# Performance work log

Hardware: AMD Instinct MI355X
Metric: run time of the kernel (lower is better)

## Reference

```python
import jax, jax.numpy as jnp
import numpy as np

B, L, D = 1, 512, 768
INIT_STD = 0.02


def setup_inputs() -> dict:
    key = jax.random.key(0)
    ks = jax.random.split(key, 6)
    hidden_states = jax.random.normal(ks[0], (B, L, D), dtype=jnp.float32)
    attention_mask = jnp.zeros((B, 1, L), dtype=jnp.float32)  # additive mask
    # nn.Linear weights, stored as [in, out] so forward is x @ W + b
    Wq = jax.random.normal(ks[1], (D, D), dtype=jnp.float32) * INIT_STD
    bq = jnp.zeros((D,), dtype=jnp.float32)
    Wk = jax.random.normal(ks[2], (D, D), dtype=jnp.float32) * INIT_STD
    bk = jnp.zeros((D,), dtype=jnp.float32)
    w_att = jax.random.normal(ks[3], (D,), dtype=jnp.float32) * INIT_STD  # Linear(D,1)
    b_att = jnp.zeros((), dtype=jnp.float32)
    Wt = jax.random.normal(ks[4], (D, D), dtype=jnp.float32) * INIT_STD
    bt = jnp.zeros((D,), dtype=jnp.float32)
    return {
        "hidden_states": hidden_states,
        "attention_mask": attention_mask,
        "Wq": Wq, "bq": bq, "Wk": Wk, "bk": bk,
        "w_att": w_att, "b_att": b_att, "Wt": Wt, "bt": bt,
    }


def reference(hidden_states, attention_mask, Wq, bq, Wk, bk, w_att, b_att, Wt, bt):
    # Additive (Bahdanau) attention
    Q = hidden_states @ Wq + bq                      # [B, L, D]
    K = hidden_states @ Wk + bk                      # [B, L, D]
    # Broadcast add -> tanh -> linear score: the O(B,L,L,D) intermediate
    feats = jnp.tanh(Q[:, :, None, :] + K[:, None, :, :])   # [B, Lq, Lk, D]
    scores = jnp.einsum('bqkd,d->bqk', feats, w_att) + b_att # [B, Lq, Lk]
    scores = scores + attention_mask                 # additive mask, broadcast
    probs = jax.nn.softmax(scores, axis=-1)          # [B, Lq, Lk]
    weighted = jnp.einsum('bqk,bkd->bqd', probs, hidden_states)  # [B, L, D]
    return weighted @ Wt + bt + Q
```

## Files before the change

kernel.cpp:

```cpp
#include <hip/hip_runtime.h>

#define L 512
#define D 768
#define LL (L * L)
#define LOG2E  1.44269504088896341f
#define LOG2E2 2.88539008177792681f
#define DH 8
#define DSEG (D / DH)
#define QB 8

typedef __attribute__((ext_vector_type(8))) short bf16x8;
typedef __attribute__((ext_vector_type(4))) short bf16x4;
typedef __attribute__((ext_vector_type(4))) float f32x4;
typedef __attribute__((ext_vector_type(2))) float f32x2;

__device__ __forceinline__ ushort f2bf(float f) {
    unsigned u = __builtin_bit_cast(unsigned, f);
    u += 0x7FFFu + ((u >> 16) & 1u);
    return (ushort)(u >> 16);
}

__device__ __forceinline__ unsigned cvt_pk(float lo, float hi) {
    unsigned r;
    asm("v_cvt_pk_bf16_f32 %0, %1, %2" : "=v"(r) : "v"(lo), "v"(hi));
    return r;
}

__device__ __forceinline__ f32x2 dup2(float x) { return (f32x2){x, x}; }

__global__ __launch_bounds__(256) void gemm_proj(
    const float* __restrict__ Xf,
    const float* __restrict__ W0, const float* __restrict__ W1,
    const float* __restrict__ W2,
    const float* __restrict__ bq, const float* __restrict__ bk,
    float* __restrict__ Qb, float* __restrict__ Eq,
    float* __restrict__ EkT, ushort* __restrict__ XWtT)
{
    const int N = D, K = D;
    const int bz = blockIdx.z;

    __shared__ __align__(16) ushort As[32][72];
    __shared__ __align__(16) ushort Bs[64][76];

    const int m0 = blockIdx.y * 32;
    const int n0 = blockIdx.x * 64;
    const int t = threadIdx.x;
    const int l = t & 63, w = t >> 6;
    const int wr = w >> 1, wc = w & 1;
    const int frow = l & 15;
    const int kg = (l >> 4) * 8;

    const float* Wm = bz == 0 ? W0 : bz == 1 ? W1 : W2;
    const int srow = t >> 3, sk = (t & 7) * 8;
    const int kq = (t >> 4) * 4, nc = (t & 15) * 4;
    const float* ApF = Xf + (m0 + srow) * D + sk;
    const float* WpF = Wm + kq * D + n0 + nc;

    float4 pa0 = *(const float4*)(ApF + 0);
    float4 pa1 = *(const float4*)(ApF + 4);
    float4 pw0 = *(const float4*)(WpF + 0 * D);
    float4 pw1 = *(const float4*)(WpF + 1 * D);
    float4 pw2 = *(const float4*)(WpF + 2 * D);
    float4 pw3 = *(const float4*)(WpF + 3 * D);

    f32x4 acc[2] = {};

    for (int k0 = 0; k0 < K; k0 += 64) {
        if (k0) __syncthreads();
        {
            uint4 av;
            av.x = cvt_pk(pa0.x, pa0.y);
            av.y = cvt_pk(pa0.z, pa0.w);
            av.z = cvt_pk(pa1.x, pa1.y);
            av.w = cvt_pk(pa1.z, pa1.w);
            *(uint4*)&As[srow][sk] = av;
        }
        {
            uint2 b;
            b.x = cvt_pk(pw0.x, pw1.x); b.y = cvt_pk(pw2.x, pw3.x);
            *(uint2*)&Bs[nc + 0][kq] = b;
            b.x = cvt_pk(pw0.y, pw1.y); b.y = cvt_pk(pw2.y, pw3.y);
            *(uint2*)&Bs[nc + 1][kq] = b;
            b.x = cvt_pk(pw0.z, pw1.z); b.y = cvt_pk(pw2.z, pw3.z);
            *(uint2*)&Bs[nc + 2][kq] = b;
            b.x = cvt_pk(pw0.w, pw1.w); b.y = cvt_pk(pw2.w, pw3.w);
            *(uint2*)&Bs[nc + 3][kq] = b;
        }
        __syncthreads();
        if (k0 + 64 < K) {
            pa0 = *(const float4*)(ApF + k0 + 64);
            pa1 = *(const float4*)(ApF + k0 + 68);
            pw0 = *(const float4*)(WpF + (k0 + 64) * D);
            pw1 = *(const float4*)(WpF + (k0 + 65) * D);
            pw2 = *(const float4*)(WpF + (k0 + 66) * D);
            pw3 = *(const float4*)(WpF + (k0 + 67) * D);
        }

        bf16x8 af[2];
        #pragma unroll
        for (int kk = 0; kk < 2; ++kk)
            af[kk] = *(const bf16x8*)&As[16 * wr + frow][32 * kk + kg];
        #pragma unroll
        for (int fc = 0; fc < 2; ++fc)
            #pragma unroll
            for (int kk = 0; kk < 2; ++kk) {
                bf16x4 lo = *(const bf16x4*)&Bs[32 * wc + 16 * fc + frow][32 * kk + kg];
                bf16x4 hi = *(const bf16x4*)&Bs[32 * wc + 16 * fc + frow][32 * kk + kg + 4];
                bf16x8 bv = __builtin_shufflevector(lo, hi, 0, 1, 2, 3, 4, 5, 6, 7);
                acc[fc] = __builtin_amdgcn_mfma_f32_16x16x32_bf16(af[kk], bv, acc[fc], 0, 0, 0);
            }
    }

    const int rg = (l >> 4) * 4;
    #pragma unroll
    for (int fc = 0; fc < 2; ++fc) {
        const int col = n0 + 32 * wc + 16 * fc + frow;
        const int row0 = m0 + 16 * wr + rg;
        if (bz == 2) {
            uint2 e;
            e.x = cvt_pk(acc[fc][0], acc[fc][1]);
            e.y = cvt_pk(acc[fc][2], acc[fc][3]);
            *(uint2*)&XWtT[col * L + row0] = e;
        } else if (bz == 1) {
            const float bv = bk[col];
            float4 e;
            e.x = __builtin_amdgcn_exp2f(LOG2E2 * (acc[fc][0] + bv));
            e.y = __builtin_amdgcn_exp2f(LOG2E2 * (acc[fc][1] + bv));
            e.z = __builtin_amdgcn_exp2f(LOG2E2 * (acc[fc][2] + bv));
            e.w = __builtin_amdgcn_exp2f(LOG2E2 * (acc[fc][3] + bv));
            *(float4*)&EkT[col * L + row0] = e;
        } else {
            const float bv = bq[col];
            #pragma unroll
            for (int i = 0; i < 4; ++i) {
                float v = acc[fc][i] + bv;
                Qb[(row0 + i) * N + col] = v;
                Eq[(row0 + i) * N + col] = __builtin_amdgcn_exp2f(LOG2E2 * v);
            }
        }
    }
}

__global__ __launch_bounds__(512) void gemm_pv(
    const ushort* __restrict__ Pbf, const ushort* __restrict__ XWtT,
    const float* __restrict__ bt, const float* __restrict__ Qb,
    float* __restrict__ out)
{
    const int N = D, K = L;
    __shared__ __align__(16) ushort As[32][72];
    __shared__ __align__(16) ushort Bs[64][72];

    const int m0 = blockIdx.y * 32;
    const int n0 = blockIdx.x * 64;
    const int t = threadIdx.x;
    const int l = t & 63, w = t >> 6;
    const int wr = w >> 2, wc = w & 3;
    const int frow = l & 15;
    const int kg = (l >> 4) * 8;

    const int srA = t >> 4, skA = (t & 15) * 4;
    const int srB = t >> 3, skB = (t & 7) * 8;
    const ushort* Ap = Pbf  + (m0 + srA) * K + skA;
    const ushort* Bp = XWtT + (n0 + srB) * K + skB;

    uint2 a0 = *(const uint2*)Ap;
    uint4 b0 = *(const uint4*)Bp;

    f32x4 acc = {};

    for (int k0 = 0; k0 < K; k0 += 64) {
        if (k0) __syncthreads();
        *(uint2*)&As[srA][skA] = a0;
        *(uint4*)&Bs[srB][skB] = b0;
        __syncthreads();
        if (k0 + 64 < K) {
            a0 = *(const uint2*)(Ap + k0 + 64);
            b0 = *(const uint4*)(Bp + k0 + 64);
        }
        #pragma unroll
        for (int kk = 0; kk < 2; ++kk) {
            bf16x8 af = *(const bf16x8*)&As[16 * wr + frow][32 * kk + kg];
            bf16x8 bv = *(const bf16x8*)&Bs[16 * wc + frow][32 * kk + kg];
            acc = __builtin_amdgcn_mfma_f32_16x16x32_bf16(af, bv, acc, 0, 0, 0);
        }
    }

    const int rg = (l >> 4) * 4;
    const int col = n0 + 16 * wc + frow;
    const int row0 = m0 + 16 * wr + rg;
    const float bv = bt[col];
    #pragma unroll
    for (int i = 0; i < 4; ++i)
        out[(row0 + i) * N + col] = acc[i] + bv + Qb[(row0 + i) * N + col];
}

__global__ __launch_bounds__(256) void score_k(
    const float* __restrict__ Eq, const float* __restrict__ EkT,
    const float* __restrict__ w_att, float* __restrict__ sP)
{
    __shared__ __align__(16) float eqlds[DSEG][8];
    __shared__ __align__(16) float wlds[DSEG];
    const int kt = blockIdx.x;
    const int dh = blockIdx.y;
    const int qg = blockIdx.z;
    const int q0 = qg * QB;
    const int dbase = dh * DSEG;
    const int tid = threadIdx.x;
    const int lane = tid & 63, wv = tid >> 6;
    const int k = kt * 256 + wv * 64 + lane;

    {
        const int row = tid >> 5;
        const int j   = tid & 31;
        #pragma unroll
        for (int c = 0; c < 3; ++c) {
            int d = j + 32 * c;
            eqlds[d][row] = Eq[(q0 + row) * D + dbase + d];
        }
        if (tid < 32) {
            #pragma unroll
            for (int c = 0; c < 3; ++c) {
                int d = tid + 32 * c;
                wlds[d] = (-2.f * LOG2E) * w_att[dbase + d];
            }
        }
    }
    __syncthreads();

    const float* __restrict__ ekp = EkT + dbase * L + k;
    const f32x2 one = dup2(1.f);
    f32x2 acc2[4] = {};

    #pragma unroll 2
    for (int d0 = 0; d0 < DSEG; d0 += 4) {
        f32x2 ek0 = dup2(ekp[(d0 + 0) * L]);
        f32x2 ek1 = dup2(ekp[(d0 + 1) * L]);
        f32x2 ek2 = dup2(ekp[(d0 + 2) * L]);
        f32x2 ek3 = dup2(ekp[(d0 + 3) * L]);
        f32x4 wq4 = *(const f32x4*)&wlds[d0];
        f32x2 w0 = dup2(wq4[0]), w1 = dup2(wq4[1]);
        f32x2 w2 = dup2(wq4[2]), w3 = dup2(wq4[3]);
        f32x4 Elo[4], Ehi[4];
        #pragma unroll
        for (int dd = 0; dd < 4; ++dd) {
            Elo[dd] = *(const f32x4*)&eqlds[d0 + dd][0];
            Ehi[dd] = *(const f32x4*)&eqlds[d0 + dd][4];
        }
        #pragma unroll
        for (int j = 0; j < 4; ++j) {
            #define GET2(dd) ((j < 2) ? (f32x2){Elo[dd][2 * j], Elo[dd][2 * j + 1]} \
                                      : (f32x2){Ehi[dd][2 * j - 4], Ehi[dd][2 * j - 3]})
            f32x2 e0 = GET2(0);
            f32x2 e1 = GET2(1);
            f32x2 e2 = GET2(2);
            f32x2 e3 = GET2(3);
            #undef GET2
            f32x2 Aa = __builtin_elementwise_fma(e0, ek0, one);
            f32x2 Bb = __builtin_elementwise_fma(e1, ek1, one);
            f32x2 Cc = __builtin_elementwise_fma(e2, ek2, one);
            f32x2 Dd = __builtin_elementwise_fma(e3, ek3, one);
            f32x2 AB = Aa * Bb, CD = Cc * Dd;
            f32x2 N1 = __builtin_elementwise_fma(w0, Bb, w1 * Aa);
            f32x2 N2 = __builtin_elementwise_fma(w2, Dd, w3 * Cc);
            f32x2 Nm = __builtin_elementwise_fma(N1, CD, N2 * AB);
            f32x2 P = AB * CD;
            f32x2 R;
            R.x = __builtin_amdgcn_rcpf(P.x);
            R.y = __builtin_amdgcn_rcpf(P.y);
            acc2[j] = __builtin_elementwise_fma(Nm, R, acc2[j]);
        }
    }

    float* __restrict__ dst = sP + dh * LL + q0 * L + k;
    #pragma unroll
    for (int j = 0; j < 4; ++j) {
        dst[(2 * j + 0) * L] = acc2[j].x;
        dst[(2 * j + 1) * L] = acc2[j].y;
    }
}

__global__ __launch_bounds__(512) void softmax_probs(
    const float* __restrict__ sP, const float* __restrict__ mask,
    ushort* __restrict__ Pbf)
{
    __shared__ float redB[8];
    const int q = blockIdx.x;
    const int tid = threadIdx.x;
    const int lane = tid & 63, wave = tid >> 6;

    float v = LOG2E * mask[tid];
    #pragma unroll
    for (int h = 0; h < DH; ++h)
        v += sP[h * LL + q * L + tid];

    float e = __builtin_amdgcn_exp2f(v);
    float s = e;
    #pragma unroll
    for (int off = 32; off; off >>= 1)
        s += __shfl_xor(s, off);
    if (lane == 0) redB[wave] = s;
    __syncthreads();
    float t0 = redB[0];
    #pragma unroll
    for (int i = 1; i < 8; ++i) t0 += redB[i];
    Pbf[q * L + tid] = f2bf(e * __builtin_amdgcn_rcpf(t0));
}

extern "C" void kernel_launch(void* const* d_in, const int* in_sizes, int n_in,
                              void* d_out, int out_size, void* d_ws, size_t ws_size,
                              hipStream_t stream) {
    const float* X     = (const float*)d_in[0];
    const float* mask  = (const float*)d_in[1];
    const float* Wq    = (const float*)d_in[2];
    const float* bq    = (const float*)d_in[3];
    const float* Wk    = (const float*)d_in[4];
    const float* bk    = (const float*)d_in[5];
    const float* w_att = (const float*)d_in[6];
    const float* Wt    = (const float*)d_in[8];
    const float* bt    = (const float*)d_in[9];
    float* out = (float*)d_out;

    const int LD = L * D;
    float*  Qb   = (float*)d_ws;
    float*  Eq   = Qb + LD;
    float*  EkT  = Eq + LD;
    float*  sP   = EkT + LD;
    ushort* XWtT = (ushort*)(sP + DH * LL);
    ushort* Pbf  = XWtT + LD;

    gemm_proj<<<dim3(D / 64, L / 32, 3), 256, 0, stream>>>(
        X, Wq, Wk, Wt, bq, bk, Qb, Eq, EkT, XWtT);

    score_k<<<dim3(2, DH, L / QB), 256, 0, stream>>>(Eq, EkT, w_att, sP);

    softmax_probs<<<dim3(L), 512, 0, stream>>>(sP, mask, Pbf);

    gemm_pv<<<dim3(D / 64, L / 32), 512, 0, stream>>>(Pbf, XWtT, bt, Qb, out);
}
```

Measured before the change: 45.79 us.

## Fuse score and softmax kernels and store exp(K) in bf16

Merges the split-D score kernel and the softmax kernel into one kernel where each block computes full-D scores for two queries across all keys and applies the masked softmax in place. This removes the large partial-score buffer round trip and one launch. exp(2K) is stored in bf16 to halve its read traffic. In exchange, each Ek load is reused across fewer queries, per-thread loops are longer with a single accumulator chain, and Ek precision drops.

```diff
diff --git a/kernel.cpp b/kernel.cpp
--- a/kernel.cpp
+++ b/kernel.cpp
@@ -5,9 +5,6 @@
 #define LL (L * L)
 #define LOG2E  1.44269504088896341f
 #define LOG2E2 2.88539008177792681f
-#define DH 8
-#define DSEG (D / DH)
-#define QB 8
 
 typedef __attribute__((ext_vector_type(8))) short bf16x8;
 typedef __attribute__((ext_vector_type(4))) short bf16x4;
@@ -18,6 +15,10 @@
     unsigned u = __builtin_bit_cast(unsigned, f);
     u += 0x7FFFu + ((u >> 16) & 1u);
     return (ushort)(u >> 16);
+}
+
+__device__ __forceinline__ float bf2f(ushort u) {
+    return __builtin_bit_cast(float, (unsigned)u << 16);
 }
 
 __device__ __forceinline__ unsigned cvt_pk(float lo, float hi) {
@@ -34,7 +35,7 @@
     const float* __restrict__ W2,
     const float* __restrict__ bq, const float* __restrict__ bk,
     float* __restrict__ Qb, float* __restrict__ Eq,
-    float* __restrict__ EkT, ushort* __restrict__ XWtT)
+    ushort* __restrict__ EkTb, ushort* __restrict__ XWtT)
 {
     const int N = D, K = D;
     const int bz = blockIdx.z;
@@ -123,12 +124,14 @@
             *(uint2*)&XWtT[col * L + row0] = e;
         } else if (bz == 1) {
             const float bv = bk[col];
-            float4 e;
-            e.x = __builtin_amdgcn_exp2f(LOG2E2 * (acc[fc][0] + bv));
-            e.y = __builtin_amdgcn_exp2f(LOG2E2 * (acc[fc][1] + bv));
-            e.z = __builtin_amdgcn_exp2f(LOG2E2 * (acc[fc][2] + bv));
-            e.w = __builtin_amdgcn_exp2f(LOG2E2 * (acc[fc][3] + bv));
-            *(float4*)&EkT[col * L + row0] = e;
+            float e0 = __builtin_amdgcn_exp2f(LOG2E2 * (acc[fc][0] + bv));
+            float e1 = __builtin_amdgcn_exp2f(LOG2E2 * (acc[fc][1] + bv));
+            float e2 = __builtin_amdgcn_exp2f(LOG2E2 * (acc[fc][2] + bv));
+            float e3 = __builtin_amdgcn_exp2f(LOG2E2 * (acc[fc][3] + bv));
+            uint2 e;
+            e.x = cvt_pk(e0, e1);
+            e.y = cvt_pk(e2, e3);
+            *(uint2*)&EkTb[col * L + row0] = e;
         } else {
             const float bv = bq[col];
             #pragma unroll
@@ -141,6 +144,79 @@
     }
 }
 
+__global__ __launch_bounds__(512) void score_softmax(
+    const float* __restrict__ Eq, const ushort* __restrict__ EkTb,
+    const float* __restrict__ w_att, const float* __restrict__ mask,
+    ushort* __restrict__ Pbf)
+{
+    __shared__ __align__(16) float eqlds[D][2];
+    __shared__ __align__(16) float wlds[D];
+    __shared__ float redA[8], redB[8];
+
+    const int q0 = blockIdx.x * 2;
+    const int tid = threadIdx.x;
+    const int lane = tid & 63, wave = tid >> 6;
+    const int k = tid;
+
+    for (int i = tid; i < D; i += 512) {
+        eqlds[i][0] = Eq[q0 * D + i];
+        eqlds[i][1] = Eq[(q0 + 1) * D + i];
+        wlds[i] = (-2.f * LOG2E) * w_att[i];
+    }
+    __syncthreads();
+
+    const ushort* __restrict__ ekp = EkTb + k;
+    const f32x2 one = dup2(1.f);
+    f32x2 acc2 = {};
+
+    #pragma unroll 4
+    for (int d0 = 0; d0 < D; d0 += 4) {
+        f32x2 ek0 = dup2(bf2f(ekp[(d0 + 0) * L]));
+        f32x2 ek1 = dup2(bf2f(ekp[(d0 + 1) * L]));
+        f32x2 ek2 = dup2(bf2f(ekp[(d0 + 2) * L]));
+        f32x2 ek3 = dup2(bf2f(ekp[(d0 + 3) * L]));
+        f32x4 wq4 = *(const f32x4*)&wlds[d0];
+        f32x2 w0 = dup2(wq4[0]), w1 = dup2(wq4[1]);
+        f32x2 w2 = dup2(wq4[2]), w3 = dup2(wq4[3]);
+        f32x2 e0 = *(const f32x2*)&eqlds[d0 + 0][0];
+        f32x2 e1 = *(const f32x2*)&eqlds[d0 + 1][0];
+        f32x2 e2 = *(const f32x2*)&eqlds[d0 + 2][0];
+        f32x2 e3 = *(const f32x2*)&eqlds[d0 + 3][0];
+        f32x2 Aa = __builtin_elementwise_fma(e0, ek0, one);
+        f32x2 Bb = __builtin_elementwise_fma(e1, ek1, one);
+        f32x2 Cc = __builtin_elementwise_fma(e2, ek2, one);
+        f32x2 Dd = __builtin_elementwise_fma(e3, ek3, one);
+        f32x2 AB = Aa * Bb, CD = Cc * Dd;
+        f32x2 N1 = __builtin_elementwise_fma(w0, Bb, w1 * Aa);
+        f32x2 N2 = __builtin_elementwise_fma(w2, Dd, w3 * Cc);
+        f32x2 Nm = __builtin_elementwise_fma(N1, CD, N2 * AB);
+        f32x2 P = AB * CD;
+        f32x2 R;
+        R.x = __builtin_amdgcn_rcpf(P.x);
+        R.y = __builtin_amdgcn_rcpf(P.y);
+        acc2 = __builtin_elementwise_fma(Nm, R, acc2);
+    }
+
+    const float mk = LOG2E * mask[k];
+    float e0 = __builtin_amdgcn_exp2f(acc2.x + mk);
+    float e1 = __builtin_amdgcn_exp2f(acc2.y + mk);
+
+    float s0 = e0, s1 = e1;
+    #pragma unroll
+    for (int off = 32; off; off >>= 1) {
+        s0 += __shfl_xor(s0, off);
+        s1 += __shfl_xor(s1, off);
+    }
+    if (lane == 0) { redA[wave] = s0; redB[wave] = s1; }
+    __syncthreads();
+    float t0 = redA[0], t1 = redB[0];
+    #pragma unroll
+    for (int i = 1; i < 8; ++i) { t0 += redA[i]; t1 += redB[i]; }
+
+    Pbf[q0 * L + k]       = f2bf(e0 * __builtin_amdgcn_rcpf(t0));
+    Pbf[(q0 + 1) * L + k] = f2bf(e1 * __builtin_amdgcn_rcpf(t1));
+}
+
 __global__ __launch_bounds__(512) void gemm_pv(
     const ushort* __restrict__ Pbf, const ushort* __restrict__ XWtT,
     const float* __restrict__ bt, const float* __restrict__ Qb,
@@ -192,118 +268,6 @@
     #pragma unroll
     for (int i = 0; i < 4; ++i)
         out[(row0 + i) * N + col] = acc[i] + bv + Qb[(row0 + i) * N + col];
-}
-
-__global__ __launch_bounds__(256) void score_k(
-    const float* __restrict__ Eq, const float* __restrict__ EkT,
-    const float* __restrict__ w_att, float* __restrict__ sP)
-{
-    __shared__ __align__(16) float eqlds[DSEG][8];
-    __shared__ __align__(16) float wlds[DSEG];
-    const int kt = blockIdx.x;
-    const int dh = blockIdx.y;
-    const int qg = blockIdx.z;
-    const int q0 = qg * QB;
-    const int dbase = dh * DSEG;
-    const int tid = threadIdx.x;
-    const int lane = tid & 63, wv = tid >> 6;
-    const int k = kt * 256 + wv * 64 + lane;
-
-    {
-        const int row = tid >> 5;
-        const int j   = tid & 31;
-        #pragma unroll
-        for (int c = 0; c < 3; ++c) {
-            int d = j + 32 * c;
-            eqlds[d][row] = Eq[(q0 + row) * D + dbase + d];
-        }
-        if (tid < 32) {
-            #pragma unroll
-            for (int c = 0; c < 3; ++c) {
-                int d = tid + 32 * c;
-                wlds[d] = (-2.f * LOG2E) * w_att[dbase + d];
-            }
-        }
-    }
-    __syncthreads();
-
-    const float* __restrict__ ekp = EkT + dbase * L + k;
-    const f32x2 one = dup2(1.f);
-    f32x2 acc2[4] = {};
-
-    #pragma unroll 2
-    for (int d0 = 0; d0 < DSEG; d0 += 4) {
-        f32x2 ek0 = dup2(ekp[(d0 + 0) * L]);
-        f32x2 ek1 = dup2(ekp[(d0 + 1) * L]);
-        f32x2 ek2 = dup2(ekp[(d0 + 2) * L]);
-        f32x2 ek3 = dup2(ekp[(d0 + 3) * L]);
-        f32x4 wq4 = *(const f32x4*)&wlds[d0];
-        f32x2 w0 = dup2(wq4[0]), w1 = dup2(wq4[1]);
-        f32x2 w2 = dup2(wq4[2]), w3 = dup2(wq4[3]);
-        f32x4 Elo[4], Ehi[4];
-        #pragma unroll
-        for (int dd = 0; dd < 4; ++dd) {
-            Elo[dd] = *(const f32x4*)&eqlds[d0 + dd][0];
-            Ehi[dd] = *(const f32x4*)&eqlds[d0 + dd][4];
-        }
-        #pragma unroll
-        for (int j = 0; j < 4; ++j) {
-            #define GET2(dd) ((j < 2) ? (f32x2){Elo[dd][2 * j], Elo[dd][2 * j + 1]} \
-                                      : (f32x2){Ehi[dd][2 * j - 4], Ehi[dd][2 * j - 3]})
-            f32x2 e0 = GET2(0);
-            f32x2 e1 = GET2(1);
-            f32x2 e2 = GET2(2);
-            f32x2 e3 = GET2(3);
-            #undef GET2
-            f32x2 Aa = __builtin_elementwise_fma(e0, ek0, one);
-            f32x2 Bb = __builtin_elementwise_fma(e1, ek1, one);
-            f32x2 Cc = __builtin_elementwise_fma(e2, ek2, one);
-            f32x2 Dd = __builtin_elementwise_fma(e3, ek3, one);
-            f32x2 AB = Aa * Bb, CD = Cc * Dd;
-            f32x2 N1 = __builtin_elementwise_fma(w0, Bb, w1 * Aa);
-            f32x2 N2 = __builtin_elementwise_fma(w2, Dd, w3 * Cc);
-            f32x2 Nm = __builtin_elementwise_fma(N1, CD, N2 * AB);
-            f32x2 P = AB * CD;
-            f32x2 R;
-            R.x = __builtin_amdgcn_rcpf(P.x);
-            R.y = __builtin_amdgcn_rcpf(P.y);
-            acc2[j] = __builtin_elementwise_fma(Nm, R, acc2[j]);
-        }
-    }
-
-    float* __restrict__ dst = sP + dh * LL + q0 * L + k;
-    #pragma unroll
-    for (int j = 0; j < 4; ++j) {
-        dst[(2 * j + 0) * L] = acc2[j].x;
-        dst[(2 * j + 1) * L] = acc2[j].y;
-    }
-}
-
-__global__ __launch_bounds__(512) void softmax_probs(
-    const float* __restrict__ sP, const float* __restrict__ mask,
-    ushort* __restrict__ Pbf)
-{
-    __shared__ float redB[8];
-    const int q = blockIdx.x;
-    const int tid = threadIdx.x;
-    const int lane = tid & 63, wave = tid >> 6;
-
-    float v = LOG2E * mask[tid];
-    #pragma unroll
-    for (int h = 0; h < DH; ++h)
-        v += sP[h * LL + q * L + tid];
-
-    float e = __builtin_amdgcn_exp2f(v);
-    float s = e;
-    #pragma unroll
-    for (int off = 32; off; off >>= 1)
-        s += __shfl_xor(s, off);
-    if (lane == 0) redB[wave] = s;
-    __syncthreads();
-    float t0 = redB[0];
-    #pragma unroll
-    for (int i = 1; i < 8; ++i) t0 += redB[i];
-    Pbf[q * L + tid] = f2bf(e * __builtin_amdgcn_rcpf(t0));
 }
 
 extern "C" void kernel_launch(void* const* d_in, const int* in_sizes, int n_in,
@@ -323,17 +287,14 @@
     const int LD = L * D;
     float*  Qb   = (float*)d_ws;
     float*  Eq   = Qb + LD;
-    float*  EkT  = Eq + LD;
-    float*  sP   = EkT + LD;
-    ushort* XWtT = (ushort*)(sP + DH * LL);
+    ushort* EkTb = (ushort*)(Eq + LD);
+    ushort* XWtT = EkTb + LD;
     ushort* Pbf  = XWtT + LD;
 
     gemm_proj<<<dim3(D / 64, L / 32, 3), 256, 0, stream>>>(
-        X, Wq, Wk, Wt, bq, bk, Qb, Eq, EkT, XWtT);
-
-    score_k<<<dim3(2, DH, L / QB), 256, 0, stream>>>(Eq, EkT, w_att, sP);
-
-    softmax_probs<<<dim3(L), 512, 0, stream>>>(sP, mask, Pbf);
+        X, Wq, Wk, Wt, bq, bk, Qb, Eq, EkTb, XWtT);
+
+    score_softmax<<<dim3(L / 2), 512, 0, stream>>>(Eq, EkTb, w_att, mask, Pbf);
 
     gemm_pv<<<dim3(D / 64, L / 32), 512, 0, stream>>>(Pbf, XWtT, bt, Qb, out);
 }
```

Result: slower. 51.10 us (+11.6%).
